# Kernel optimization log

Measured on AMD Instinct MI355X. Metric: run time of the kernel, lower is better.

## Reference

```python
import jax, jax.numpy as jnp
import numpy as np

K = 3
PAD = 1


def _conv_offset(x, w_off, b_off):
    # standard 3x3 conv, stride 1, pad 1, with bias -> [B, 18, H, W]
    y = jax.lax.conv_general_dilated(
        x, w_off, window_strides=(1, 1), padding=((PAD, PAD), (PAD, PAD)),
        dimension_numbers=('NCHW', 'OIHW', 'NCHW'))
    return y + b_off[None, :, None, None]


def _deform_conv(x, offset, w_dcn):
    # x: [B,Cin,H,W], offset: [B,2*K*K,H,W] (dy,dx interleaved per tap), w_dcn: [Cout,Cin,K,K]
    B, Cin, H, W = x.shape
    KK = K * K
    Ho, Wo = offset.shape[2], offset.shape[3]

    ky = jnp.repeat(jnp.arange(K), K)          # [KK] kernel row index
    kx = jnp.tile(jnp.arange(K), K)            # [KK] kernel col index
    off = offset.reshape(B, KK, 2, Ho, Wo)
    dy, dx = off[:, :, 0], off[:, :, 1]        # [B,KK,Ho,Wo]

    gy = (jnp.arange(Ho)[None, :, None] - PAD + ky[:, None, None]).astype(x.dtype)  # [KK,Ho,1]
    gx = (jnp.arange(Wo)[None, None, :] - PAD + kx[:, None, None]).astype(x.dtype)  # [KK,1,Wo]
    py = gy[None] + dy                         # [B,KK,Ho,Wo] sampling rows
    px = gx[None] + dx                         # [B,KK,Ho,Wo] sampling cols

    y0 = jnp.floor(py); x0 = jnp.floor(px)
    wy1 = py - y0; wx1 = px - x0
    wy0 = 1.0 - wy1; wx0 = 1.0 - wx1

    x_flat = x.reshape(B, Cin, H * W)

    def gather(yi, xi, wgt):
        valid = (yi >= 0) & (yi <= H - 1) & (xi >= 0) & (xi <= W - 1)
        yc = jnp.clip(yi, 0, H - 1).astype(jnp.int32)
        xc = jnp.clip(xi, 0, W - 1).astype(jnp.int32)
        idx = yc * W + xc                      # [B,KK,Ho,Wo]
        vals = jax.vmap(lambda xb, ib: xb[:, ib])(x_flat, idx)  # [B,Cin,KK,Ho,Wo]
        w = (wgt * valid.astype(x.dtype))[:, None]              # [B,1,KK,Ho,Wo]
        return vals * w

    sampled = (gather(y0, x0, wy0 * wx0)
               + gather(y0, x0 + 1, wy0 * wx1)
               + gather(y0 + 1, x0, wy1 * wx0)
               + gather(y0 + 1, x0 + 1, wy1 * wx1))  # [B,Cin,KK,Ho,Wo]

    wr = w_dcn.reshape(w_dcn.shape[0], Cin, KK)
    return jnp.einsum('bckhw,ock->bohw', sampled, wr)


def setup_inputs() -> dict:
    key = jax.random.key(0)
    k1, k2, k3, k4 = jax.random.split(key, 4)
    B, Cin, H, W = 8, 32, 160, 160
    Cout = 32
    x = jax.random.normal(k1, (B, Cin, H, W), jnp.float32)
    w_off = jax.random.normal(k2, (2 * K * K, Cin, K, K), jnp.float32) * 0.01
    b_off = jax.random.normal(k3, (2 * K * K,), jnp.float32) * 0.01
    w_dcn = jax.random.normal(k4, (Cout, Cin, K, K), jnp.float32) * 0.1
    return {'x': x, 'w_off': w_off, 'b_off': b_off, 'w_dcn': w_dcn}


def reference(x, w_off, b_off, w_dcn):
    offset = _conv_offset(x, w_off, b_off)
    y = _deform_conv(x, offset, w_dcn)
    return jax.nn.relu(y)
```

## Files before the change

kernel.cpp:

```cpp
#include <hip/hip_runtime.h>

#define H_ 160
#define W_ 160
#define HW_ (H_ * W_)
#define NPIX (8 * HW_)


typedef __attribute__((ext_vector_type(8)))  short  short8;
typedef __attribute__((ext_vector_type(4)))  float  f32x4;
typedef __attribute__((ext_vector_type(2)))  float  f32x2;
typedef __attribute__((ext_vector_type(16))) float  f32x16;
typedef __attribute__((ext_vector_type(4)))  unsigned u32x4;

__device__ __forceinline__ unsigned short bf16_rne(float f) {
    unsigned u = __float_as_uint(f);
    u += 0x7fffu + ((u >> 16) & 1u);
    return (unsigned short)(u >> 16);
}
__device__ __forceinline__ unsigned pack2_bf16(float a, float b) {
    unsigned ua = __float_as_uint(a); ua += 0x7fffu + ((ua >> 16) & 1u);
    unsigned ub = __float_as_uint(b); ub += 0x7fffu + ((ub >> 16) & 1u);
    return (ua >> 16) | (ub & 0xffff0000u);
}
__device__ __forceinline__ f32x2 up2(unsigned u) {
    f32x2 r;
    r.x = __uint_as_float(u << 16);
    r.y = __uint_as_float(u & 0xffff0000u);
    return r;
}

__global__ __launch_bounds__(256) void nhwc_bf16(
    const float* __restrict__ x, unsigned short* __restrict__ xT)
{
    const int pix = blockIdx.x * 256 + threadIdx.x;
    const int p = pix % HW_;
    const int b = pix / HW_;
    const float* __restrict__ src = x + (size_t)b * 32 * HW_ + p;
    unsigned* __restrict__ dst = (unsigned*)(xT + (size_t)pix * 32);
    #pragma unroll
    for (int g = 0; g < 16; ++g)
        dst[g] = pack2_bf16(src[(2 * g) * HW_], src[(2 * g + 1) * HW_]);
}

__global__ __launch_bounds__(256, 3) void dcn_fused(
    const unsigned short* __restrict__ xT,
    const float* __restrict__ w_off,
    const float* __restrict__ b_off,
    const float* __restrict__ w_dcn,
    float* __restrict__ out)
{
    __shared__ __align__(16) unsigned short wo[9 * 2 * 64 * 8];
    __shared__ __align__(16) unsigned short wd[9 * 2 * 64 * 8];
    __shared__ float offl[4 * 18 * 33];
    __shared__ float bl[32];
    const int tid = threadIdx.x;
    for (int d = tid; d < 9 * 1024; d += 256) {
        const int tap = d >> 10, r = d & 1023, j = r >> 5, c = r & 31;
        const int s = c >> 4, kg = (c >> 3) & 1;
        const int unit = (tap * 2 + s) * 64 + j + 32 * kg;
        wo[unit * 8 + (c & 7)] = (j < 18) ? bf16_rne(w_off[(j * 32 + c) * 9 + tap])
                                          : (unsigned short)0;
        wd[unit * 8 + (c & 7)] = bf16_rne(w_dcn[(j * 32 + c) * 9 + tap]);
    }
    if (tid < 32) bl[tid] = (tid < 18) ? b_off[tid] : 0.0f;
    __syncthreads();

    const int wave = tid >> 6, lane = tid & 63;
    const int n = lane & 31;
    const int hh = lane >> 5;
    const int pixbase = blockIdx.x * 128 + wave * 32;
    const int pix = pixbase + n;
    const int w = pix % W_, h = (pix / W_) % H_, b = pix / HW_;
    const unsigned short* __restrict__ xb = xT + (size_t)b * HW_ * 32 + hh * 8;

    {
        f32x16 acc = {};
        const u32x4 z4 = {0u, 0u, 0u, 0u};
        #pragma unroll
        for (int tap = 0; tap < 9; ++tap) {
            const int yy = h - 1 + tap / 3;
            const int xx = w - 1 + tap % 3;
            const bool valid = (yy >= 0) && (yy < H_) && (xx >= 0) && (xx < W_);
            const int idx = min(max(yy, 0), H_ - 1) * W_ + min(max(xx, 0), W_ - 1);
            const unsigned short* __restrict__ px_ = xb + (size_t)idx * 32;
            u32x4 l0 = *(const u32x4*)(px_);
            u32x4 l1 = *(const u32x4*)(px_ + 16);
            l0 = valid ? l0 : z4;
            l1 = valid ? l1 : z4;
            const short8 a0 = __builtin_bit_cast(short8, l0);
            const short8 a1 = __builtin_bit_cast(short8, l1);
            const short8 b0 = *(const short8*)(wo + ((tap * 2 + 0) * 64 + lane) * 8);
            const short8 b1 = *(const short8*)(wo + ((tap * 2 + 1) * 64 + lane) * 8);
            acc = __builtin_amdgcn_mfma_f32_32x32x16_bf16(a0, b0, acc, 0, 0, 0);
            acc = __builtin_amdgcn_mfma_f32_32x32x16_bf16(a1, b1, acc, 0, 0, 0);
        }
        float* __restrict__ owp = offl + wave * 594;
        if (n < 18) {
            const float bia = bl[n];
            #pragma unroll
            for (int r = 0; r < 16; ++r) {
                const int prow = (r & 3) + 8 * (r >> 2) + 4 * hh;
                owp[n * 33 + prow] = acc[r] + bia;
            }
        }
    }
    __syncthreads();

    const float* __restrict__ ow = offl + wave * 594;
    f32x16 acc = {};

    #pragma unroll
    for (int tap = 0; tap < 9; ++tap) {
        const float dy = ow[(2 * tap) * 33 + n];
        const float dx = ow[(2 * tap + 1) * 33 + n];
        const float py = (float)(h - 1 + tap / 3) + dy;
        const float px = (float)(w - 1 + tap % 3) + dx;
        const float fy0 = floorf(py), fx0 = floorf(px);
        const float wy1 = py - fy0, wx1 = px - fx0;
        const float wy0 = 1.0f - wy1, wx0 = 1.0f - wx1;
        const int y0 = (int)fy0, x0 = (int)fx0;
        const bool vy0 = (y0 >= 0) && (y0 < H_);
        const bool vy1 = (y0 + 1 >= 0) && (y0 + 1 < H_);
        const bool vx0 = (x0 >= 0) && (x0 < W_);
        const bool vx1 = (x0 + 1 >= 0) && (x0 + 1 < W_);
        const float w00 = (vy0 && vx0) ? wy0 * wx0 : 0.0f;
        const float w01 = (vy0 && vx1) ? wy0 * wx1 : 0.0f;
        const float w10 = (vy1 && vx0) ? wy1 * wx0 : 0.0f;
        const float w11 = (vy1 && vx1) ? wy1 * wx1 : 0.0f;
        const int yc0 = min(max(y0, 0), H_ - 1), yc1 = min(max(y0 + 1, 0), H_ - 1);
        const int xc0 = min(max(x0, 0), W_ - 1), xc1 = min(max(x0 + 1, 0), W_ - 1);

        const unsigned short* __restrict__ pA = xb + (size_t)(yc0 * W_ + xc0) * 32;
        const unsigned short* __restrict__ pB = xb + (size_t)(yc0 * W_ + xc1) * 32;
        const unsigned short* __restrict__ pC = xb + (size_t)(yc1 * W_ + xc0) * 32;
        const unsigned short* __restrict__ pD = xb + (size_t)(yc1 * W_ + xc1) * 32;
        const u32x4 A0 = *(const u32x4*)(pA);      const u32x4 A1 = *(const u32x4*)(pA + 16);
        const u32x4 B0 = *(const u32x4*)(pB);      const u32x4 B1 = *(const u32x4*)(pB + 16);
        const u32x4 C0 = *(const u32x4*)(pC);      const u32x4 C1 = *(const u32x4*)(pC + 16);
        const u32x4 D0 = *(const u32x4*)(pD);      const u32x4 D1 = *(const u32x4*)(pD + 16);

        #define COMB(a, bb, cc, dd) ({ \
            const f32x2 v = up2(a) * w00 + up2(bb) * w01 + up2(cc) * w10 + up2(dd) * w11; \
            pack2_bf16(v.x, v.y); })
        u32x4 av0, av1;
        av0.x = COMB(A0.x, B0.x, C0.x, D0.x);
        av0.y = COMB(A0.y, B0.y, C0.y, D0.y);
        av0.z = COMB(A0.z, B0.z, C0.z, D0.z);
        av0.w = COMB(A0.w, B0.w, C0.w, D0.w);
        av1.x = COMB(A1.x, B1.x, C1.x, D1.x);
        av1.y = COMB(A1.y, B1.y, C1.y, D1.y);
        av1.z = COMB(A1.z, B1.z, C1.z, D1.z);
        av1.w = COMB(A1.w, B1.w, C1.w, D1.w);
        #undef COMB

        const short8 a0 = __builtin_bit_cast(short8, av0);
        const short8 a1 = __builtin_bit_cast(short8, av1);
        const short8 b0 = *(const short8*)(wd + ((tap * 2 + 0) * 64 + lane) * 8);
        const short8 b1 = *(const short8*)(wd + ((tap * 2 + 1) * 64 + lane) * 8);
        acc = __builtin_amdgcn_mfma_f32_32x32x16_bf16(a0, b0, acc, 0, 0, 0);
        acc = __builtin_amdgcn_mfma_f32_32x32x16_bf16(a1, b1, acc, 0, 0, 0);
    }

    float* __restrict__ ob = out + (size_t)b * 32 * HW_ + (size_t)n * HW_
                           + (pixbase - b * HW_) + 4 * hh;
    #pragma unroll
    for (int g = 0; g < 4; ++g) {
        f32x4 r;
        #pragma unroll
        for (int i = 0; i < 4; ++i) r[i] = fmaxf(acc[g * 4 + i], 0.0f);
        *(f32x4*)(ob + g * 8) = r;
    }
}

extern "C" void kernel_launch(void* const* d_in, const int* in_sizes, int n_in,
                              void* d_out, int out_size, void* d_ws, size_t ws_size,
                              hipStream_t stream) {
    const float* x     = (const float*)d_in[0];
    const float* w_off = (const float*)d_in[1];
    const float* b_off = (const float*)d_in[2];
    const float* w_dcn = (const float*)d_in[3];
    float* out = (float*)d_out;

    unsigned short* xT = (unsigned short*)d_ws;

    nhwc_bf16<<<800, 256, 0, stream>>>(x, xT);
    dcn_fused<<<1600, 256, 0, stream>>>(xT, w_off, b_off, w_dcn, out);
}
```

Baseline: 157.9 us.

## Share one LDS weight buffer between offset and deform phases to raise occupancy

Replaces the two separate LDS weight arrays with a single buffer. It holds the offset-conv weights first and is then overwritten with the deform-conv weights after an extra barrier. Weight staging now packs eight bf16 values per thread into 16-byte LDS stores, and the offset results are written back with vectorized float4 stores. Launch bounds rise from 3 to 5 blocks per CU to use the freed LDS, but this adds a second barrier and reloads the weights in every block.

```diff
diff --git a/kernel.cpp b/kernel.cpp
--- a/kernel.cpp
+++ b/kernel.cpp
@@ -42,25 +42,32 @@
         dst[g] = pack2_bf16(src[(2 * g) * HW_], src[(2 * g + 1) * HW_]);
 }
 
-__global__ __launch_bounds__(256, 3) void dcn_fused(
+__global__ __launch_bounds__(256, 5) void dcn_fused(
     const unsigned short* __restrict__ xT,
     const float* __restrict__ w_off,
     const float* __restrict__ b_off,
     const float* __restrict__ w_dcn,
     float* __restrict__ out)
 {
-    __shared__ __align__(16) unsigned short wo[9 * 2 * 64 * 8];
-    __shared__ __align__(16) unsigned short wd[9 * 2 * 64 * 8];
-    __shared__ float offl[4 * 18 * 33];
+    __shared__ __align__(16) unsigned short wsh[9 * 128 * 8];
+    __shared__ float offl[4 * 594];
     __shared__ float bl[32];
     const int tid = threadIdx.x;
-    for (int d = tid; d < 9 * 1024; d += 256) {
-        const int tap = d >> 10, r = d & 1023, j = r >> 5, c = r & 31;
-        const int s = c >> 4, kg = (c >> 3) & 1;
-        const int unit = (tap * 2 + s) * 64 + j + 32 * kg;
-        wo[unit * 8 + (c & 7)] = (j < 18) ? bf16_rne(w_off[(j * 32 + c) * 9 + tap])
-                                          : (unsigned short)0;
-        wd[unit * 8 + (c & 7)] = bf16_rne(w_dcn[(j * 32 + c) * 9 + tap]);
+
+    for (int u = tid; u < 1152; u += 256) {
+        const int tap = u >> 7, rem = u & 127;
+        const int s = rem >> 6, rem2 = rem & 63;
+        const int kg = rem2 >> 5, col = rem2 & 31;
+        const int cb = s * 16 + kg * 8;
+        u32x4 v = {0u, 0u, 0u, 0u};
+        if (col < 18) {
+            const float* __restrict__ wp = w_off + (size_t)(col * 32 + cb) * 9 + tap;
+            v.x = pack2_bf16(wp[0 * 9], wp[1 * 9]);
+            v.y = pack2_bf16(wp[2 * 9], wp[3 * 9]);
+            v.z = pack2_bf16(wp[4 * 9], wp[5 * 9]);
+            v.w = pack2_bf16(wp[6 * 9], wp[7 * 9]);
+        }
+        *(u32x4*)(wsh + u * 8) = v;
     }
     if (tid < 32) bl[tid] = (tid < 18) ? b_off[tid] : 0.0f;
     __syncthreads();
@@ -89,8 +96,8 @@
             l1 = valid ? l1 : z4;
             const short8 a0 = __builtin_bit_cast(short8, l0);
             const short8 a1 = __builtin_bit_cast(short8, l1);
-            const short8 b0 = *(const short8*)(wo + ((tap * 2 + 0) * 64 + lane) * 8);
-            const short8 b1 = *(const short8*)(wo + ((tap * 2 + 1) * 64 + lane) * 8);
+            const short8 b0 = *(const short8*)(wsh + ((tap * 2 + 0) * 64 + lane) * 8);
+            const short8 b1 = *(const short8*)(wsh + ((tap * 2 + 1) * 64 + lane) * 8);
             acc = __builtin_amdgcn_mfma_f32_32x32x16_bf16(a0, b0, acc, 0, 0, 0);
             acc = __builtin_amdgcn_mfma_f32_32x32x16_bf16(a1, b1, acc, 0, 0, 0);
         }
@@ -98,11 +105,28 @@
         if (n < 18) {
             const float bia = bl[n];
             #pragma unroll
-            for (int r = 0; r < 16; ++r) {
-                const int prow = (r & 3) + 8 * (r >> 2) + 4 * hh;
-                owp[n * 33 + prow] = acc[r] + bia;
+            for (int g = 0; g < 4; ++g) {
+                f32x4 r;
+                #pragma unroll
+                for (int i = 0; i < 4; ++i) r[i] = acc[g * 4 + i] + bia;
+                *(f32x4*)(owp + n * 33 + 8 * g + 4 * hh) = r;
             }
         }
+    }
+    __syncthreads();
+
+    for (int u = tid; u < 1152; u += 256) {
+        const int tap = u >> 7, rem = u & 127;
+        const int s = rem >> 6, rem2 = rem & 63;
+        const int kg = rem2 >> 5, col = rem2 & 31;
+        const int cb = s * 16 + kg * 8;
+        const float* __restrict__ wp = w_dcn + (size_t)(col * 32 + cb) * 9 + tap;
+        u32x4 v;
+        v.x = pack2_bf16(wp[0 * 9], wp[1 * 9]);
+        v.y = pack2_bf16(wp[2 * 9], wp[3 * 9]);
+        v.z = pack2_bf16(wp[4 * 9], wp[5 * 9]);
+        v.w = pack2_bf16(wp[6 * 9], wp[7 * 9]);
+        *(u32x4*)(wsh + u * 8) = v;
     }
     __syncthreads();
 
@@ -155,8 +179,8 @@
 
         const short8 a0 = __builtin_bit_cast(short8, av0);
         const short8 a1 = __builtin_bit_cast(short8, av1);
-        const short8 b0 = *(const short8*)(wd + ((tap * 2 + 0) * 64 + lane) * 8);
-        const short8 b1 = *(const short8*)(wd + ((tap * 2 + 1) * 64 + lane) * 8);
+        const short8 b0 = *(const short8*)(wsh + ((tap * 2 + 0) * 64 + lane) * 8);
+        const short8 b1 = *(const short8*)(wsh + ((tap * 2 + 1) * 64 + lane) * 8);
         acc = __builtin_amdgcn_mfma_f32_32x32x16_bf16(a0, b0, acc, 0, 0, 0);
         acc = __builtin_amdgcn_mfma_f32_32x32x16_bf16(a1, b1, acc, 0, 0, 0);
     }
```

After: 177.2 us. 12.2% more time.
